# Kernel tuning notes

Hardware: AMD Instinct MI355X
Metric: run time of the kernel (lower is better)

Reference implementation:

```python
import jax, jax.numpy as jnp
import numpy as np

NUM_HEADS = 16


def setup_inputs() -> dict:
    key = jax.random.key(0)
    k1, k2, k3 = jax.random.split(key, 3)
    B, N, C = 4, 2048, 1024
    x = jax.random.normal(k1, (B, N, C), dtype=jnp.float32)
    qkv_w = jax.random.normal(k2, (3 * C, C), dtype=jnp.float32) * (C ** -0.5)
    proj_w = jax.random.normal(k3, (C, C), dtype=jnp.float32) * (C ** -0.5)
    proj_b = jnp.zeros((C,), dtype=jnp.float32)
    return {"x": x, "qkv_w": qkv_w, "proj_w": proj_w, "proj_b": proj_b, "len_t": 256}


def reference(x, qkv_w, proj_w, proj_b, len_t):
    B, N, C = x.shape
    H = NUM_HEADS
    hd = C // H
    scale = hd ** -0.5
    # qkv: [B, N, 3C] -> [3, B, H, N, hd]
    qkv = (x @ qkv_w.T).reshape(B, N, 3, H, hd).transpose(2, 0, 3, 1, 4)
    q, k, v = qkv[0], qkv[1], qkv[2]
    q_s = q[:, :, len_t:]                      # [B, H, N-len_t, hd] partial queries
    attn = jnp.einsum('bhqd,bhkd->bhqk', q_s, k) * scale
    attn = jax.nn.softmax(attn, axis=-1)       # [B, H, N-len_t, N]
    x_s = jnp.einsum('bhqk,bhkd->bhqd', attn, v)
    x_s = x_s.transpose(0, 2, 1, 3).reshape(B, N - len_t, C)
    x_t = x[:, :len_t]                         # template tokens pass through
    x_out = jnp.concatenate((x_t, x_s), axis=1)
    return x_out @ proj_w.T + proj_b
```

## Files before the change

### kernel.cpp

```cpp
#include <hip/hip_runtime.h>
#include <stdint.h>

typedef unsigned short u16;
typedef __attribute__((ext_vector_type(4))) short short4v;
typedef __attribute__((ext_vector_type(8))) short short8;
typedef __attribute__((ext_vector_type(4))) float floatx4;
typedef __attribute__((ext_vector_type(4))) unsigned short u16x4;

typedef __attribute__((address_space(1))) const void* gas_ptr;
typedef __attribute__((address_space(3))) void* las_ptr;

__device__ __forceinline__ void async16(const void* g, void* l) {
    __builtin_amdgcn_global_load_lds((gas_ptr)g, (las_ptr)l, 16, 0, 0);
}

__device__ __forceinline__ u16 f2bf(float f) {
    union { float f; unsigned int u; } v; v.f = f;
    unsigned int r = v.u + 0x7fffu + ((v.u >> 16) & 1u);
    return (u16)(r >> 16);
}

__device__ __forceinline__ int pk_bf16(float a, float b) {
    return (int)((unsigned int)f2bf(a) | ((unsigned int)f2bf(b) << 16));
}

__device__ __forceinline__ int pk2t(float a, float b) {
    union { float f; unsigned int u; } ua, ub;
    ua.f = a; ub.f = b;
    return (int)__builtin_amdgcn_perm(ub.u, ua.u, 0x07060302u);
}

__global__ void cvt_w_kernel(const float* __restrict__ src, u16* __restrict__ dst) {
    int i = blockIdx.x * 256 + threadIdx.x;
    float4 f = reinterpret_cast<const float4*>(src)[i];
    u16x4 o;
    o.x = f2bf(f.x); o.y = f2bf(f.y); o.z = f2bf(f.z); o.w = f2bf(f.w);
    reinterpret_cast<u16x4*>(dst)[i] = o;
}

__global__ void cvt_x_kernel(const float* __restrict__ x, u16* __restrict__ xb,
                             u16* __restrict__ xout) {
    int i = blockIdx.x * 256 + threadIdx.x;
    float4 f = reinterpret_cast<const float4*>(x)[i];
    u16x4 o;
    o.x = f2bf(f.x); o.y = f2bf(f.y); o.z = f2bf(f.z); o.w = f2bf(f.w);
    reinterpret_cast<u16x4*>(xb)[i] = o;
    int m = (i * 4) >> 10;
    if ((m & 2047) < 256) reinterpret_cast<u16x4*>(xout)[i] = o;
}

__global__ void __launch_bounds__(512, 2)
gemm_qkv(const u16* __restrict__ A, const u16* __restrict__ B,
         u16* __restrict__ q_out, u16* __restrict__ k_out, u16* __restrict__ vt_out) {
    __shared__ u16 As[3][256 * 32];
    __shared__ u16 Bs[3][192 * 32];
    const int tid  = threadIdx.x;
    const int lane = tid & 63;
    const int w    = tid >> 6;
    const int wr   = w >> 2;
    const int wc   = w & 3;
    const int row0 = blockIdx.x * 256;
    const int col0 = blockIdx.y * 192;
    const int m    = lane & 15;
    const int g    = lane >> 4;

    floatx4 acc[8][3] = {};

#define STAGE_A8(buf, kelem)                                                    \
    do {                                                                        \
        _Pragma("unroll")                                                       \
        for (int i = 0; i < 2; ++i) {                                           \
            int p = tid + i * 512;                                              \
            int r = p >> 2;                                                     \
            int c = (p & 3) ^ ((r >> 1) & 3);                                   \
            async16(A + (size_t)(row0 + r) * 1024 + ((kelem) + c * 8),          \
                    (char*)&As[buf][0] + p * 16);                               \
        }                                                                       \
    } while (0)

#define STAGE_B8(buf, kelem)                                                    \
    do {                                                                        \
        _Pragma("unroll")                                                       \
        for (int i = 0; i < 2; ++i) {                                           \
            int p = (i == 0) ? tid : (tid + 256);                               \
            int r = p >> 2;                                                     \
            int c = (p & 3) ^ ((r >> 1) & 3);                                   \
            async16(B + (size_t)(col0 + r) * 1024 + ((kelem) + c * 8),          \
                    (char*)&Bs[buf][0] + p * 16);                               \
        }                                                                       \
    } while (0)

    STAGE_A8(0, 0);  STAGE_B8(0, 0);
    STAGE_A8(1, 32); STAGE_B8(1, 32);

    int cur = 0, nx2 = 2;
    for (int kt = 0; kt < 32; ++kt) {
        if (kt < 31) asm volatile("s_waitcnt vmcnt(4)" ::: "memory");
        else         asm volatile("s_waitcnt vmcnt(0)" ::: "memory");
        __builtin_amdgcn_s_barrier();

        const u16* as = &As[cur][0];
        const u16* bs = &Bs[cur][0];
        short8 af[8], bf[3];
#pragma unroll
        for (int j = 0; j < 3; ++j) {
            int br = wc * 48 + j * 16 + m;
            bf[j] = *(const short8*)(bs + br * 32 + (g ^ ((br >> 1) & 3)) * 8);
        }
#pragma unroll
        for (int i = 0; i < 4; ++i) {
            int ar = wr * 128 + i * 16 + m;
            af[i] = *(const short8*)(as + ar * 32 + (g ^ ((ar >> 1) & 3)) * 8);
        }
        if (kt + 2 < 32) STAGE_A8(nx2, (kt + 2) * 32);
        __builtin_amdgcn_s_setprio(1);
#pragma unroll
        for (int i = 0; i < 4; ++i)
#pragma unroll
            for (int j = 0; j < 3; ++j)
                acc[i][j] = __builtin_amdgcn_mfma_f32_16x16x32_bf16(af[i], bf[j], acc[i][j], 0, 0, 0);
        __builtin_amdgcn_s_setprio(0);
        __builtin_amdgcn_s_barrier();
#pragma unroll
        for (int i = 4; i < 8; ++i) {
            int ar = wr * 128 + i * 16 + m;
            af[i] = *(const short8*)(as + ar * 32 + (g ^ ((ar >> 1) & 3)) * 8);
        }
        if (kt + 2 < 32) STAGE_B8(nx2, (kt + 2) * 32);
        __builtin_amdgcn_s_setprio(1);
#pragma unroll
        for (int i = 4; i < 8; ++i)
#pragma unroll
            for (int j = 0; j < 3; ++j)
                acc[i][j] = __builtin_amdgcn_mfma_f32_16x16x32_bf16(af[i], bf[j], acc[i][j], 0, 0, 0);
        __builtin_amdgcn_s_setprio(0);

        cur = (cur == 2) ? 0 : cur + 1;
        nx2 = (nx2 == 2) ? 0 : nx2 + 1;
    }
#undef STAGE_A8
#undef STAGE_B8

#pragma unroll
    for (int i = 0; i < 8; ++i) {
#pragma unroll
        for (int j = 0; j < 3; ++j) {
            int gr0 = row0 + wr * 128 + i * 16 + (g << 2);
            int gc  = col0 + wc * 48 + j * 16 + m;
            int which = gc >> 10;
            int cl = gc & 1023;
            int h = cl >> 6, d = cl & 63;
            int b = gr0 >> 11, n0 = gr0 & 2047;
            int bh = b * 16 + h;
            if (which == 2) {
                u16x4 pk;
                pk.x = f2bf(acc[i][j][0]); pk.y = f2bf(acc[i][j][1]);
                pk.z = f2bf(acc[i][j][2]); pk.w = f2bf(acc[i][j][3]);
                size_t off = (size_t)bh * 131072
                           + (((size_t)(n0 >> 5) * 4 + (d >> 4)) * 64
                              + ((n0 >> 3) & 3) * 16 + (d & 15)) * 8 + (n0 & 4);
                *reinterpret_cast<u16x4*>(vt_out + off) = pk;
            } else {
                u16* dst = (which == 0) ? q_out : k_out;
                float sc = (which == 0) ? 0.18033688f : 1.0f;
#pragma unroll
                for (int r = 0; r < 4; ++r)
                    dst[((size_t)bh * 2048 + n0 + r) * 64 + d] = f2bf(acc[i][j][r] * sc);
            }
        }
    }
}

template<int MODE>
__global__ void __launch_bounds__(256, 2)
gemm_nt(const u16* __restrict__ A, const u16* __restrict__ B,
        float* __restrict__ f_out, const float* __restrict__ bias, int K) {
    __shared__ u16 As[3][128 * 32];
    __shared__ u16 Bs[3][128 * 32];
    const int tid  = threadIdx.x;
    const int lane = tid & 63;
    const int w    = tid >> 6;
    const int row0 = blockIdx.x * 128;
    const int col0 = blockIdx.y * 128;
    const int wm   = (w >> 1) * 64;
    const int wn   = (w & 1) * 64;

    floatx4 acc[4][4] = {};

#define STAGE_G(buf, kelem)                                                     \
    do {                                                                        \
        _Pragma("unroll")                                                       \
        for (int i = 0; i < 2; ++i) {                                           \
            int pb = w * 128 + i * 64;                                          \
            int p  = pb + lane;                                                 \
            int r  = p >> 2;                                                    \
            int c  = (p & 3) ^ ((r >> 1) & 3);                                  \
            async16(A + (size_t)(row0 + r) * K + ((kelem) + c * 8),             \
                    (char*)&As[buf][0] + p * 16);                               \
            async16(B + (size_t)(col0 + r) * K + ((kelem) + c * 8),             \
                    (char*)&Bs[buf][0] + p * 16);                               \
        }                                                                       \
    } while (0)

    STAGE_G(0, 0);
    STAGE_G(1, 32);
    const int nk = K >> 5;

    int cur = 0;
    int nx2 = 2;
    for (int kt = 0; kt < nk; ++kt) {
        if (kt + 1 < nk) {
            asm volatile("s_waitcnt vmcnt(4)" ::: "memory");
        } else {
            asm volatile("s_waitcnt vmcnt(0)" ::: "memory");
        }
        __builtin_amdgcn_s_barrier();
        __builtin_amdgcn_sched_barrier(0);
        if (kt + 2 < nk) STAGE_G(nx2, (kt + 2) << 5);

        const u16* as = &As[cur][0];
        const u16* bs = &Bs[cur][0];
        short8 af[4], bf_[4];
#pragma unroll
        for (int t = 0; t < 4; ++t) {
            int ar = wm + t * 16 + (lane & 15);
            int ca = (lane >> 4) ^ ((ar >> 1) & 3);
            af[t]  = *(const short8*)(as + ar * 32 + ca * 8);
            int br = wn + t * 16 + (lane & 15);
            int cb = (lane >> 4) ^ ((br >> 1) & 3);
            bf_[t] = *(const short8*)(bs + br * 32 + cb * 8);
        }
#pragma unroll
        for (int i = 0; i < 4; ++i)
#pragma unroll
            for (int j = 0; j < 4; ++j)
                acc[i][j] = __builtin_amdgcn_mfma_f32_16x16x32_bf16(af[i], bf_[j], acc[i][j], 0, 0, 0);

        cur = (cur == 2) ? 0 : cur + 1;
        nx2 = (nx2 == 2) ? 0 : nx2 + 1;
    }
#undef STAGE_G

#pragma unroll
    for (int i = 0; i < 4; ++i) {
#pragma unroll
        for (int j = 0; j < 4; ++j) {
            int gr0 = row0 + wm + i * 16 + ((lane >> 4) << 2);
            int gc  = col0 + wn + j * 16 + (lane & 15);
            float bv = bias[gc];
#pragma unroll
            for (int r = 0; r < 4; ++r)
                f_out[(size_t)(gr0 + r) * 1024 + gc] = acc[i][j][r] + bv;
        }
    }
}

__global__ void __launch_bounds__(256, 3)
flash_attn(const u16* __restrict__ Qg, const u16* __restrict__ Kg,
           const u16* __restrict__ Vf, u16* __restrict__ xout) {
    __shared__ u16 Ks[2][64 * 64];
    __shared__ u16 Vs[2][8 * 512];
    const int lane = threadIdx.x & 63;
    const int w    = threadIdx.x >> 6;
    const int bh   = blockIdx.x & 63;
    const int qt   = blockIdx.x >> 6;
    const int q0   = 256 + qt * 128 + w * 32;
    const size_t kvbase = (size_t)bh * 2048 * 64;

    const int m = lane & 15;
    const int g = lane >> 4;

    short8 qf[2][2];
#pragma unroll
    for (int qs = 0; qs < 2; ++qs) {
        const u16* p = Qg + kvbase + (size_t)(q0 + qs * 16 + m) * 64 + g * 8;
        qf[qs][0] = *(const short8*)(p);
        qf[qs][1] = *(const short8*)(p + 32);
    }

    const u16* vg = Vf + (size_t)bh * 131072;

    const int p0 = w * 64 + lane;
    const int tid = threadIdx.x;
#define STAGE_KV(buf, kt)                                                       \
    {                                                                           \
        _Pragma("unroll")                                                       \
        for (int i = 0; i < 2; ++i) {                                           \
            int p = i * 256 + p0;                                               \
            int r = p >> 3;                                                     \
            int c = (p & 7) ^ ((((r >> 3) & 1) << 2) | (r & 3));                \
            async16(Kg + kvbase + (size_t)((kt) * 64 + r) * 64 + c * 8,         \
                    (char*)&Ks[buf][0] + p * 16);                               \
        }                                                                       \
        _Pragma("unroll")                                                       \
        for (int i = 0; i < 2; ++i) {                                           \
            int p = i * 256 + tid;                                              \
            async16(vg + (size_t)((kt) * 8 + (p >> 6)) * 512 + (p & 63) * 8,    \
                    (char*)&Vs[buf][0] + p * 16);                               \
        }                                                                       \
    }

    STAGE_KV(0, 0);

    const floatx4 ZROW = {-32.f, -32.f, -32.f, -32.f};
    short8 ones1;
#pragma unroll
    for (int i = 0; i < 8; ++i) ones1[i] = (short)0x3F80;

    floatx4 lacc[2] = {};
    floatx4 o[2][4] = {};

    const int fm = ((m >> 2) & 1) * 4 + (m & 3);

    for (int kt = 0; kt < 32; ++kt) {
        __syncthreads();
        if (kt + 1 < 32) STAGE_KV((kt + 1) & 1, kt + 1);

        const u16* kbuf = &Ks[kt & 1][0];
        const u16* vbuf = &Vs[kt & 1][0];
#pragma unroll
        for (int b32 = 0; b32 < 2; ++b32) {
            short8 vfr[4];
#pragma unroll
            for (int i = 0; i < 4; ++i)
                vfr[i] = *(const short8*)(vbuf + ((b32 * 4 + i) * 64 + lane) * 8);

            floatx4 sT[2][2];
#pragma unroll
            for (int t = 0; t < 2; ++t) {
                int r = b32 * 32 + (m >> 2) * 8 + t * 4 + (m & 3);
                short8 k0 = *(const short8*)(kbuf + r * 64 + ((g)     ^ fm) * 8);
                short8 k1 = *(const short8*)(kbuf + r * 64 + ((4 + g) ^ fm) * 8);
                __builtin_amdgcn_s_setprio(1);
#pragma unroll
                for (int qs = 0; qs < 2; ++qs) {
                    floatx4 z = __builtin_amdgcn_mfma_f32_16x16x32_bf16(k0, qf[qs][0], ZROW, 0, 0, 0);
                    sT[qs][t] = __builtin_amdgcn_mfma_f32_16x16x32_bf16(k1, qf[qs][1], z, 0, 0, 0);
                }
                __builtin_amdgcn_s_setprio(0);
            }

#pragma unroll
            for (int qs = 0; qs < 2; ++qs) {
                float p[8];
#pragma unroll
                for (int t = 0; t < 2; ++t)
#pragma unroll
                    for (int r = 0; r < 4; ++r)
                        p[t * 4 + r] = __builtin_amdgcn_exp2f(sT[qs][t][r]);
                union { int i4[4]; short8 s8; } u;
                u.i4[0] = pk2t(p[0], p[1]);
                u.i4[1] = pk2t(p[2], p[3]);
                u.i4[2] = pk2t(p[4], p[5]);
                u.i4[3] = pk2t(p[6], p[7]);
                __builtin_amdgcn_s_setprio(1);
#pragma unroll
                for (int i = 0; i < 4; ++i)
                    o[qs][i] = __builtin_amdgcn_mfma_f32_16x16x32_bf16(vfr[i], u.s8, o[qs][i], 0, 0, 0);
                lacc[qs] = __builtin_amdgcn_mfma_f32_16x16x32_bf16(ones1, u.s8, lacc[qs], 0, 0, 0);
                __builtin_amdgcn_s_setprio(0);
            }
        }
    }

    const int b = bh >> 4, h = bh & 15;
#pragma unroll
    for (int qs = 0; qs < 2; ++qs) {
        const float inv = 1.f / lacc[qs][0];

        const int n = q0 + qs * 16 + m;
        u16* dst = xout + (size_t)(b * 2048 + n) * 1024 + h * 64 + (g << 2);
#pragma unroll
        for (int i = 0; i < 4; ++i) {
            union { int i2[2]; u16x4 s4; } u;
            u.i2[0] = pk_bf16(o[qs][i][0] * inv, o[qs][i][1] * inv);
            u.i2[1] = pk_bf16(o[qs][i][2] * inv, o[qs][i][3] * inv);
            *reinterpret_cast<u16x4*>(dst + i * 16) = u.s4;
        }
    }
#undef STAGE_KV
}

extern "C" void kernel_launch(void* const* d_in, const int* in_sizes, int n_in,
                              void* d_out, int out_size, void* d_ws, size_t ws_size,
                              hipStream_t stream) {
    const float* x      = (const float*)d_in[0];
    const float* qkv_w  = (const float*)d_in[1];
    const float* proj_w = (const float*)d_in[2];
    const float* proj_b = (const float*)d_in[3];

    char* ws = (char*)d_ws;
    u16* xb    = (u16*)(ws);
    u16* xout  = (u16*)(ws + ((size_t)16 << 20));
    u16* wqkv  = (u16*)(ws + ((size_t)32 << 20));
    u16* wproj = (u16*)(ws + ((size_t)38 << 20));
    u16* Qb    = (u16*)(ws + ((size_t)40 << 20));
    u16* Kb    = (u16*)(ws + ((size_t)56 << 20));
    u16* Vfb   = (u16*)(ws + ((size_t)72 << 20));

    cvt_x_kernel<<<8192, 256, 0, stream>>>(x, xb, xout);
    cvt_w_kernel<<<3072, 256, 0, stream>>>(qkv_w, wqkv);
    cvt_w_kernel<<<1024, 256, 0, stream>>>(proj_w, wproj);
    gemm_qkv<<<dim3(32, 16), 512, 0, stream>>>(xb, wqkv, Qb, Kb, Vfb);
    flash_attn<<<896, 256, 0, stream>>>(Qb, Kb, Vfb, xout);
    gemm_nt<1><<<dim3(64, 8), 256, 0, stream>>>(xout, wproj, (float*)d_out, proj_b, 1024);
}
```

Before: 255.9 us.

## Merge conversion kernels, retile projection GEMM to 256x128, raise attention occupancy

```diff
diff --git a/kernel.cpp b/kernel.cpp
--- a/kernel.cpp
+++ b/kernel.cpp
@@ -30,23 +30,25 @@
     return (int)__builtin_amdgcn_perm(ub.u, ua.u, 0x07060302u);
 }
 
-__global__ void cvt_w_kernel(const float* __restrict__ src, u16* __restrict__ dst) {
-    int i = blockIdx.x * 256 + threadIdx.x;
+__global__ void cvt_all(const float* __restrict__ x, u16* __restrict__ xb,
+                        u16* __restrict__ xout,
+                        const float* __restrict__ qkv_w, u16* __restrict__ wqkv,
+                        const float* __restrict__ proj_w, u16* __restrict__ wproj) {
+    int b = blockIdx.x;
+    const float* src;
+    u16* dst;
+    int i;
+    if (b < 8192)       { src = x;      dst = xb;    i = b * 256 + threadIdx.x; }
+    else if (b < 11264) { src = qkv_w;  dst = wqkv;  i = (b - 8192) * 256 + threadIdx.x; }
+    else                { src = proj_w; dst = wproj; i = (b - 11264) * 256 + threadIdx.x; }
     float4 f = reinterpret_cast<const float4*>(src)[i];
     u16x4 o;
     o.x = f2bf(f.x); o.y = f2bf(f.y); o.z = f2bf(f.z); o.w = f2bf(f.w);
     reinterpret_cast<u16x4*>(dst)[i] = o;
-}
-
-__global__ void cvt_x_kernel(const float* __restrict__ x, u16* __restrict__ xb,
-                             u16* __restrict__ xout) {
-    int i = blockIdx.x * 256 + threadIdx.x;
-    float4 f = reinterpret_cast<const float4*>(x)[i];
-    u16x4 o;
-    o.x = f2bf(f.x); o.y = f2bf(f.y); o.z = f2bf(f.z); o.w = f2bf(f.w);
-    reinterpret_cast<u16x4*>(xb)[i] = o;
-    int m = (i * 4) >> 10;
-    if ((m & 2047) < 256) reinterpret_cast<u16x4*>(xout)[i] = o;
+    if (b < 8192) {
+        int m = (i * 4) >> 10;
+        if ((m & 2047) < 256) reinterpret_cast<u16x4*>(xout)[i] = o;
+    }
 }
 
 __global__ void __launch_bounds__(512, 2)
@@ -171,82 +173,101 @@
     }
 }
 
-template<int MODE>
-__global__ void __launch_bounds__(256, 2)
-gemm_nt(const u16* __restrict__ A, const u16* __restrict__ B,
-        float* __restrict__ f_out, const float* __restrict__ bias, int K) {
-    __shared__ u16 As[3][128 * 32];
+__global__ void __launch_bounds__(512, 2)
+gemm_proj(const u16* __restrict__ A, const u16* __restrict__ B,
+          float* __restrict__ f_out, const float* __restrict__ bias) {
+    __shared__ u16 As[3][256 * 32];
     __shared__ u16 Bs[3][128 * 32];
     const int tid  = threadIdx.x;
     const int lane = tid & 63;
     const int w    = tid >> 6;
-    const int row0 = blockIdx.x * 128;
+    const int wr   = w >> 2;
+    const int wc   = w & 3;
+    const int row0 = blockIdx.x * 256;
     const int col0 = blockIdx.y * 128;
-    const int wm   = (w >> 1) * 64;
-    const int wn   = (w & 1) * 64;
-
-    floatx4 acc[4][4] = {};
-
-#define STAGE_G(buf, kelem)                                                     \
+    const int m    = lane & 15;
+    const int g    = lane >> 4;
+
+    floatx4 acc[8][2] = {};
+
+#define STAGE_PA(buf, kelem)                                                    \
     do {                                                                        \
         _Pragma("unroll")                                                       \
         for (int i = 0; i < 2; ++i) {                                           \
-            int pb = w * 128 + i * 64;                                          \
-            int p  = pb + lane;                                                 \
-            int r  = p >> 2;                                                    \
-            int c  = (p & 3) ^ ((r >> 1) & 3);                                  \
-            async16(A + (size_t)(row0 + r) * K + ((kelem) + c * 8),             \
+            int p = tid + i * 512;                                              \
+            int r = p >> 2;                                                     \
+            int c = (p & 3) ^ ((r >> 1) & 3);                                   \
+            async16(A + (size_t)(row0 + r) * 1024 + ((kelem) + c * 8),          \
                     (char*)&As[buf][0] + p * 16);                               \
-            async16(B + (size_t)(col0 + r) * K + ((kelem) + c * 8),             \
-                    (char*)&Bs[buf][0] + p * 16);                               \
         }                                                                       \
     } while (0)
 
-    STAGE_G(0, 0);
-    STAGE_G(1, 32);
-    const int nk = K >> 5;
-
-    int cur = 0;
-    int nx2 = 2;
-    for (int kt = 0; kt < nk; ++kt) {
-        if (kt + 1 < nk) {
-            asm volatile("s_waitcnt vmcnt(4)" ::: "memory");
-        } else {
-            asm volatile("s_waitcnt vmcnt(0)" ::: "memory");
-        }
+#define STAGE_PB(buf, kelem)                                                    \
+    do {                                                                        \
+        int p = tid;                                                            \
+        int r = p >> 2;                                                         \
+        int c = (p & 3) ^ ((r >> 1) & 3);                                       \
+        async16(B + (size_t)(col0 + r) * 1024 + ((kelem) + c * 8),              \
+                (char*)&Bs[buf][0] + p * 16);                                   \
+    } while (0)
+
+    STAGE_PA(0, 0);  STAGE_PB(0, 0);
+    STAGE_PA(1, 32); STAGE_PB(1, 32);
+
+    int cur = 0, nx2 = 2;
+    for (int kt = 0; kt < 32; ++kt) {
+        if (kt < 31) asm volatile("s_waitcnt vmcnt(3)" ::: "memory");
+        else         asm volatile("s_waitcnt vmcnt(0)" ::: "memory");
         __builtin_amdgcn_s_barrier();
-        __builtin_amdgcn_sched_barrier(0);
-        if (kt + 2 < nk) STAGE_G(nx2, (kt + 2) << 5);
 
         const u16* as = &As[cur][0];
         const u16* bs = &Bs[cur][0];
-        short8 af[4], bf_[4];
-#pragma unroll
-        for (int t = 0; t < 4; ++t) {
-            int ar = wm + t * 16 + (lane & 15);
-            int ca = (lane >> 4) ^ ((ar >> 1) & 3);
-            af[t]  = *(const short8*)(as + ar * 32 + ca * 8);
-            int br = wn + t * 16 + (lane & 15);
-            int cb = (lane >> 4) ^ ((br >> 1) & 3);
-            bf_[t] = *(const short8*)(bs + br * 32 + cb * 8);
-        }
+        short8 af[8], bf[2];
+#pragma unroll
+        for (int j = 0; j < 2; ++j) {
+            int br = wc * 32 + j * 16 + m;
+            bf[j] = *(const short8*)(bs + br * 32 + (g ^ ((br >> 1) & 3)) * 8);
+        }
+#pragma unroll
+        for (int i = 0; i < 4; ++i) {
+            int ar = wr * 128 + i * 16 + m;
+            af[i] = *(const short8*)(as + ar * 32 + (g ^ ((ar >> 1) & 3)) * 8);
+        }
+        if (kt + 2 < 32) STAGE_PA(nx2, (kt + 2) * 32);
+        __builtin_amdgcn_s_setprio(1);
 #pragma unroll
         for (int i = 0; i < 4; ++i)
 #pragma unroll
-            for (int j = 0; j < 4; ++j)
-                acc[i][j] = __builtin_amdgcn_mfma_f32_16x16x32_bf16(af[i], bf_[j], acc[i][j], 0, 0, 0);
+            for (int j = 0; j < 2; ++j)
+                acc[i][j] = __builtin_amdgcn_mfma_f32_16x16x32_bf16(af[i], bf[j], acc[i][j], 0, 0, 0);
+        __builtin_amdgcn_s_setprio(0);
+        __builtin_amdgcn_s_barrier();
+#pragma unroll
+        for (int i = 4; i < 8; ++i) {
+            int ar = wr * 128 + i * 16 + m;
+            af[i] = *(const short8*)(as + ar * 32 + (g ^ ((ar >> 1) & 3)) * 8);
+        }
+        if (kt + 2 < 32) STAGE_PB(nx2, (kt + 2) * 32);
+        __builtin_amdgcn_s_setprio(1);
+#pragma unroll
+        for (int i = 4; i < 8; ++i)
+#pragma unroll
+            for (int j = 0; j < 2; ++j)
+                acc[i][j] = __builtin_amdgcn_mfma_f32_16x16x32_bf16(af[i], bf[j], acc[i][j], 0, 0, 0);
+        __builtin_amdgcn_s_setprio(0);
 
         cur = (cur == 2) ? 0 : cur + 1;
         nx2 = (nx2 == 2) ? 0 : nx2 + 1;
     }
-#undef STAGE_G
-
-#pragma unroll
-    for (int i = 0; i < 4; ++i) {
-#pragma unroll
-        for (int j = 0; j < 4; ++j) {
-            int gr0 = row0 + wm + i * 16 + ((lane >> 4) << 2);
-            int gc  = col0 + wn + j * 16 + (lane & 15);
+#undef STAGE_PA
+#undef STAGE_PB
+
+#pragma unroll
+    for (int i = 0; i < 8; ++i) {
+#pragma unroll
+        for (int j = 0; j < 2; ++j) {
+            int gr0 = row0 + wr * 128 + i * 16 + (g << 2);
+            int gc  = col0 + wc * 32 + j * 16 + m;
             float bv = bias[gc];
 #pragma unroll
             for (int r = 0; r < 4; ++r)
@@ -255,7 +276,7 @@
     }
 }
 
-__global__ void __launch_bounds__(256, 3)
+__global__ void __launch_bounds__(256, 4)
 flash_attn(const u16* __restrict__ Qg, const u16* __restrict__ Kg,
            const u16* __restrict__ Vf, u16* __restrict__ xout) {
     __shared__ u16 Ks[2][64 * 64];
@@ -398,10 +419,8 @@
     u16* Kb    = (u16*)(ws + ((size_t)56 << 20));
     u16* Vfb   = (u16*)(ws + ((size_t)72 << 20));
 
-    cvt_x_kernel<<<8192, 256, 0, stream>>>(x, xb, xout);
-    cvt_w_kernel<<<3072, 256, 0, stream>>>(qkv_w, wqkv);
-    cvt_w_kernel<<<1024, 256, 0, stream>>>(proj_w, wproj);
+    cvt_all<<<12288, 256, 0, stream>>>(x, xb, xout, qkv_w, wqkv, proj_w, wproj);
     gemm_qkv<<<dim3(32, 16), 512, 0, stream>>>(xb, wqkv, Qb, Kb, Vfb);
     flash_attn<<<896, 256, 0, stream>>>(Qb, Kb, Vfb, xout);
-    gemm_nt<1><<<dim3(64, 8), 256, 0, stream>>>(xout, wproj, (float*)d_out, proj_b, 1024);
-}
+    gemm_proj<<<dim3(32, 8), 512, 0, stream>>>(xout, wproj, (float*)d_out, proj_b);
+}
```

Result: faster. 247.5 us (-3.3%).
